# Performance work log

Measured on AMD Instinct MI355X. Metric: run time of the kernel, lower is better.

Reference implementation:

```python
import jax, jax.numpy as jnp
import numpy as np

NEG_SLOPE = 0.2  # PyG GATConv default negative_slope


def gat_conv(x, src, dst, W, a_src, a_dst, b, concat):
    # x: [N, F_in]; src/dst: [E] edge endpoints (edge j->i means src=j, dst=i)
    N = x.shape[0]
    H, C = a_src.shape
    xp = (x @ W).reshape(N, H, C)                      # per-head projection
    al_s = jnp.einsum('nhc,hc->nh', xp, a_src)          # source attention logits
    al_d = jnp.einsum('nhc,hc->nh', xp, a_dst)          # destination attention logits
    e = jax.nn.leaky_relu(al_s[src] + al_d[dst], NEG_SLOPE)   # [E, H]
    # segment softmax over incoming edges of each destination node
    m = jax.ops.segment_max(e, dst, num_segments=N)     # [N, H]
    m = jnp.where(jnp.isfinite(m), m, jnp.zeros_like(m))
    ex = jnp.exp(e - m[dst])
    den = jax.ops.segment_sum(ex, dst, num_segments=N)  # [N, H]
    alpha = ex / (den[dst] + 1e-16)                     # [E, H]
    out = jax.ops.segment_sum(xp[src] * alpha[:, :, None], dst, num_segments=N)  # [N,H,C]
    out = out.reshape(N, H * C) if concat else out.mean(axis=1)
    return out + b


def setup_inputs() -> dict:
    key = jax.random.key(0)
    ks = jax.random.split(key, 9)
    N, E, F_in, H, C = 50000, 1600000, 128, 4, 32
    x = jax.random.normal(ks[0], (N, F_in), dtype=jnp.float32)
    edge_index = jax.random.randint(ks[1], (2, E), 0, N, dtype=jnp.int64)
    s1 = 1.0 / np.sqrt(F_in)
    s2 = 1.0 / np.sqrt(H * C)
    return {
        'x': x,
        'edge_index': edge_index,
        'W1': jax.random.normal(ks[2], (F_in, H * C), dtype=jnp.float32) * s1,
        'a_src1': jax.random.normal(ks[3], (H, C), dtype=jnp.float32) * s1,
        'a_dst1': jax.random.normal(ks[4], (H, C), dtype=jnp.float32) * s1,
        'b1': jnp.zeros((H * C,), dtype=jnp.float32),
        'W2': jax.random.normal(ks[5], (H * C, C), dtype=jnp.float32) * s2,
        'a_src2': jax.random.normal(ks[6], (1, C), dtype=jnp.float32) * s2,
        'a_dst2': jax.random.normal(ks[7], (1, C), dtype=jnp.float32) * s2,
        'b2': jnp.zeros((C,), dtype=jnp.float32),
    }


def reference(x, edge_index, W1, a_src1, a_dst1, b1, W2, a_src2, a_dst2, b2):
    N = x.shape[0]
    loops = jnp.arange(N, dtype=edge_index.dtype)
    src = jnp.concatenate([edge_index[0], loops])   # PyG default add_self_loops=True
    dst = jnp.concatenate([edge_index[1], loops])
    h = gat_conv(x, src, dst, W1, a_src1, a_dst1, b1, concat=True)
    h = jax.nn.elu(h)
    out = gat_conv(h, src, dst, W2, a_src2, a_dst2, b2, concat=False)
    return out
```

## Files before the change

### kernel.cpp

```cpp
#include <hip/hip_runtime.h>
#include <hip/hip_fp16.h>

#define NEG_SLOPE 0.2f
#define CAP 128
#define NB  64
#define GAB 192

typedef __half half_t;

__device__ __forceinline__ float lrelu(float x) { return x >= 0.f ? x : NEG_SLOPE * x; }

__device__ __forceinline__ unsigned int f2h2(float a, float b) {
    union { unsigned int u; __half2 h; } v; v.h = __floats2half2_rn(a, b);
    return v.u;
}

__device__ __forceinline__ void fma8h(const uint4& v, float w, float* a) {
    const __half* hp = (const __half*)&v;
    #pragma unroll
    for (int j = 0; j < 8; ++j) a[j] = fmaf(w, __half2float(hp[j]), a[j]);
}

__device__ __forceinline__ bool edge_is64(const int* __restrict__ ei, int E) {
    int t = threadIdx.x & 63;
    int idx = 2 * t + 1; if (idx >= 2 * E) idx = 2 * E - 1;
    unsigned long long b = __ballot(ei[idx] != 0);
    return b == 0ULL;
}

__device__ __forceinline__ void load_edge(const int* __restrict__ ei, int E, int i,
                                          bool is64, int& s, int& d) {
    if (i < E) {
        if (is64) { const long long* e = (const long long*)ei; s = (int)e[i]; d = (int)e[E + i]; }
        else      { s = ei[i]; d = ei[E + i]; }
    } else { s = d = i - E; }
}

__global__ __launch_bounds__(256) void gemm1cnt_kernel(const float* __restrict__ x,
        const float* __restrict__ W1, const float* __restrict__ a_src,
        const float* __restrict__ a_dst, half_t* __restrict__ xp1h,
        float* __restrict__ al_s, float* __restrict__ al_d,
        const int* __restrict__ ei, int* __restrict__ partials,
        unsigned int* __restrict__ epacked, int N, int E, int shift, int G1) {
    __shared__ __align__(16) float xst[64 * 128];
    __shared__ __align__(16) float ws[64 * 128];
    int t = threadIdx.x;
    if (blockIdx.x >= G1) {
        int* cnts = (int*)xst;
        int b2 = blockIdx.x - G1;
        if (t < NB) cnts[t] = 0;
        bool is64 = edge_is64(ei, E);
        __syncthreads();
        int tot = E + N;
        for (int i = b2 * 256 + t; i < tot; i += GAB * 256) {
            int s, d; load_edge(ei, E, i, is64, s, d);
            epacked[i] = ((unsigned int)d << 16) | (unsigned int)s;
            atomicAdd(&cnts[d >> shift], 1);
        }
        __syncthreads();
        if (t < NB) partials[b2 * NB + t] = cnts[t];
        return;
    }
    int row0 = blockIdx.x * 128;
    int cg = t & 15, rg = t >> 4;
    float acc[8][8] = {};
    for (int chunk = 0; chunk < 2; ++chunk) {
        __syncthreads();
        int c0 = chunk * 64;
        #pragma unroll
        for (int ii = 0; ii < 8; ++ii) {
            int idx = t + 256 * ii;
            int r = idx >> 4, kq = idx & 15;
            int n = row0 + r;
            float4 v = make_float4(0.f, 0.f, 0.f, 0.f);
            if (n < N) v = *(const float4*)&x[(size_t)n * 128 + c0 + kq * 4];
            float vv[4] = {v.x, v.y, v.z, v.w};
            #pragma unroll
            for (int j = 0; j < 4; ++j) {
                int k = kq * 4 + j;
                xst[k * 128 + (((r >> 2) ^ (k & 31)) << 2) + (r & 3)] = vv[j];
            }
        }
        #pragma unroll
        for (int ii = 0; ii < 8; ++ii) {
            int idx = t + 256 * ii;
            int k = idx >> 5, cq = idx & 31;
            *(float4*)&ws[k * 128 + cq * 4] =
                *(const float4*)&W1[(size_t)(c0 + k) * 128 + cq * 4];
        }
        __syncthreads();
        int g0 = rg * 2, g1 = rg * 2 + 1;
        #pragma unroll 4
        for (int k = 0; k < 64; ++k) {
            int kb = k & 31;
            float4 xv0 = *(const float4*)&xst[k * 128 + ((g0 ^ kb) << 2)];
            float4 xv1 = *(const float4*)&xst[k * 128 + ((g1 ^ kb) << 2)];
            float4 wv0 = *(const float4*)&ws[k * 128 + cg * 8];
            float4 wv1 = *(const float4*)&ws[k * 128 + cg * 8 + 4];
            float xr[8] = {xv0.x, xv0.y, xv0.z, xv0.w, xv1.x, xv1.y, xv1.z, xv1.w};
            float wr[8] = {wv0.x, wv0.y, wv0.z, wv0.w, wv1.x, wv1.y, wv1.z, wv1.w};
            #pragma unroll
            for (int r = 0; r < 8; ++r)
                #pragma unroll
                for (int c = 0; c < 8; ++c)
                    acc[r][c] = fmaf(xr[r], wr[c], acc[r][c]);
        }
    }
    #pragma unroll
    for (int r = 0; r < 8; ++r) {
        int n = row0 + rg * 8 + r;
        if (n < N) {
            uint4 u = make_uint4(f2h2(acc[r][0], acc[r][1]), f2h2(acc[r][2], acc[r][3]),
                                 f2h2(acc[r][4], acc[r][5]), f2h2(acc[r][6], acc[r][7]));
            *(uint4*)&xp1h[(size_t)n * 128 + cg * 8] = u;
        }
    }
    float ps[8], pd[8];
    #pragma unroll
    for (int r = 0; r < 8; ++r) {
        float s = 0.f, dd = 0.f;
        #pragma unroll
        for (int c = 0; c < 8; ++c) {
            s  = fmaf(acc[r][c], a_src[cg * 8 + c], s);
            dd = fmaf(acc[r][c], a_dst[cg * 8 + c], dd);
        }
        ps[r] = s; pd[r] = dd;
    }
    #pragma unroll
    for (int m = 1; m < 4; m <<= 1) {
        #pragma unroll
        for (int r = 0; r < 8; ++r) { ps[r] += __shfl_xor(ps[r], m); pd[r] += __shfl_xor(pd[r], m); }
    }
    if ((cg & 3) == 0) {
        int head = cg >> 2;
        #pragma unroll
        for (int r = 0; r < 8; ++r) {
            int n = row0 + rg * 8 + r;
            if (n < N) { al_s[n * 4 + head] = ps[r]; al_d[n * 4 + head] = pd[r]; }
        }
    }
}

__global__ __launch_bounds__(256) void k_bin(const unsigned int* __restrict__ epacked,
        const int* __restrict__ partials, unsigned int* __restrict__ binned,
        int tot, int shift) {
    __shared__ int cur[NB];
    int t = threadIdx.x, b = blockIdx.x;
    if (t < NB) {
        int full = 0, pre = 0;
        for (int b2 = 0; b2 < GAB; ++b2) {
            int v = partials[b2 * NB + t];
            if (b2 < b) pre += v;
            full += v;
        }
        int incl = full;
        #pragma unroll
        for (int m = 1; m < 64; m <<= 1) {
            int u = __shfl_up(incl, m);
            if (t >= m) incl += u;
        }
        cur[t] = (incl - full) + pre;
    }
    __syncthreads();
    unsigned int mask = (1u << shift) - 1u;
    for (int i = b * 256 + t; i < tot; i += GAB * 256) {
        unsigned int e = epacked[i];
        unsigned int d = e >> 16;
        int pos = atomicAdd(&cur[d >> shift], 1);
        binned[pos] = ((d & mask) << 16) | (e & 0xFFFFu);
    }
}

__global__ __launch_bounds__(1024) void k_part(const unsigned int* __restrict__ binned,
        const int* __restrict__ partials, int* __restrict__ off, int* __restrict__ csr,
        int N, int shift) {
    __shared__ int cnt_loc[1024];
    __shared__ int scan_loc[1024];
    __shared__ int wsum[16];
    __shared__ int lo_s, hi_s;
    int b = blockIdx.x, t = threadIdx.x;
    int base = b << shift;
    int span = 1 << shift;
    if (t < 64) {
        int full = 0;
        for (int b2 = 0; b2 < GAB; ++b2) full += partials[b2 * NB + t];
        int incl = full;
        #pragma unroll
        for (int m = 1; m < 64; m <<= 1) {
            int u = __shfl_up(incl, m);
            if (t >= m) incl += u;
        }
        int excl = incl - full;
        int lov = __shfl(excl, b);
        int hiv = __shfl(incl, b);
        if (t == 0) { lo_s = lov; hi_s = hiv; }
    }
    if (t < span) cnt_loc[t] = 0;
    __syncthreads();
    int lo = lo_s, hi = hi_s;
    for (int i = lo + t; i < hi; i += 1024)
        atomicAdd(&cnt_loc[binned[i] >> 16], 1);
    __syncthreads();
    int v = (t < span) ? cnt_loc[t] : 0;
    int lane = t & 63, w = t >> 6;
    int incl = v;
    #pragma unroll
    for (int m = 1; m < 64; m <<= 1) {
        int u = __shfl_up(incl, m);
        if (lane >= m) incl += u;
    }
    if (lane == 63) wsum[w] = incl;
    __syncthreads();
    if (t == 0) {
        int run = 0;
        #pragma unroll
        for (int i2 = 0; i2 < 16; ++i2) { int s2 = wsum[i2]; wsum[i2] = run; run += s2; }
    }
    __syncthreads();
    int excl = incl - v + wsum[w];
    if (t < span) { scan_loc[t] = lo + excl; off[base + t] = lo + excl; }
    __syncthreads();
    if (t < span) cnt_loc[t] = 0;
    __syncthreads();
    for (int i = lo + t; i < hi; i += 1024) {
        unsigned int e = binned[i];
        int r = e >> 16;
        int pos = scan_loc[r] + atomicAdd(&cnt_loc[r], 1);
        csr[pos] = (int)(e & 0xFFFFu);
    }
}

__global__ __launch_bounds__(256) void edge1_kernel(const int* __restrict__ off,
        const int* __restrict__ csr, const float* __restrict__ al_s,
        const float* __restrict__ al_d, const half_t* __restrict__ xp1h,
        const float* __restrict__ b1, half_t* __restrict__ h1h, int N) {
    __shared__ int   srcs[4][CAP];
    __shared__ float ew[4][CAP * 4];
    int t = threadIdx.x;
    int wid = t >> 6, lane = t & 63;
    int d = blockIdx.x * 4 + wid;
    if (d >= N) return;
    int o0 = off[d], o1 = off[d + 1];
    int deg = o1 - o0; if (deg > CAP) deg = CAP;
    float4 ad = *(const float4*)&al_d[d * 4];
    float4 ex0 = make_float4(0.f, 0.f, 0.f, 0.f);
    float4 ex1 = make_float4(0.f, 0.f, 0.f, 0.f);
    if (lane < deg) {
        int s = csr[o0 + lane];
        srcs[wid][lane] = s << 4;
        float4 as = *(const float4*)&al_s[s * 4];
        ex0.x = __expf(lrelu(as.x + ad.x));
        ex0.y = __expf(lrelu(as.y + ad.y));
        ex0.z = __expf(lrelu(as.z + ad.z));
        ex0.w = __expf(lrelu(as.w + ad.w));
    }
    if (lane + 64 < deg) {
        int s = csr[o0 + lane + 64];
        srcs[wid][lane + 64] = s << 4;
        float4 as = *(const float4*)&al_s[s * 4];
        ex1.x = __expf(lrelu(as.x + ad.x));
        ex1.y = __expf(lrelu(as.y + ad.y));
        ex1.z = __expf(lrelu(as.z + ad.z));
        ex1.w = __expf(lrelu(as.w + ad.w));
    }
    float4 r = make_float4(ex0.x + ex1.x, ex0.y + ex1.y, ex0.z + ex1.z, ex0.w + ex1.w);
    #pragma unroll
    for (int m = 1; m < 64; m <<= 1) {
        r.x += __shfl_xor(r.x, m); r.y += __shfl_xor(r.y, m);
        r.z += __shfl_xor(r.z, m); r.w += __shfl_xor(r.w, m);
    }
    float4 ri = make_float4(1.f / (r.x + 1e-16f), 1.f / (r.y + 1e-16f),
                            1.f / (r.z + 1e-16f), 1.f / (r.w + 1e-16f));
    if (lane < deg)
        *(float4*)&ew[wid][lane * 4] =
            make_float4(ex0.x * ri.x, ex0.y * ri.y, ex0.z * ri.z, ex0.w * ri.w);
    if (lane + 64 < deg)
        *(float4*)&ew[wid][(lane + 64) * 4] =
            make_float4(ex1.x * ri.x, ex1.y * ri.y, ex1.z * ri.z, ex1.w * ri.w);
    int q = lane & 15, p = lane >> 4, h = q >> 2;
    float a[8] = {};
    const uint4* xr = (const uint4*)xp1h;
    for (int ib = p; ib < deg; ib += 16) {
        int i1 = ib + 4, i2 = ib + 8, i3 = ib + 12;
        bool c1 = i1 < deg, c2 = i2 < deg, c3 = i3 < deg;
        float w0 = ew[wid][ib * 4 + h];
        uint4 v0 = xr[(size_t)(srcs[wid][ib] + q)];
        float w1, w2, w3;
        uint4 v1, v2, v3;
        if (c1) { w1 = ew[wid][i1 * 4 + h]; v1 = xr[(size_t)(srcs[wid][i1] + q)]; }
        if (c2) { w2 = ew[wid][i2 * 4 + h]; v2 = xr[(size_t)(srcs[wid][i2] + q)]; }
        if (c3) { w3 = ew[wid][i3 * 4 + h]; v3 = xr[(size_t)(srcs[wid][i3] + q)]; }
        fma8h(v0, w0, a);
        if (c1) fma8h(v1, w1, a);
        if (c2) fma8h(v2, w2, a);
        if (c3) fma8h(v3, w3, a);
    }
    #pragma unroll
    for (int j = 0; j < 8; ++j) {
        a[j] += __shfl_xor(a[j], 16);
        a[j] += __shfl_xor(a[j], 32);
    }
    if (p == 0) {
        float4 b0 = *(const float4*)&b1[q * 8];
        float4 b4 = *(const float4*)&b1[q * 8 + 4];
        float v0 = a[0] + b0.x, v1 = a[1] + b0.y, v2 = a[2] + b0.z, v3 = a[3] + b0.w;
        float v4 = a[4] + b4.x, v5 = a[5] + b4.y, v6 = a[6] + b4.z, v7 = a[7] + b4.w;
        v0 = v0 > 0.f ? v0 : expm1f(v0);
        v1 = v1 > 0.f ? v1 : expm1f(v1);
        v2 = v2 > 0.f ? v2 : expm1f(v2);
        v3 = v3 > 0.f ? v3 : expm1f(v3);
        v4 = v4 > 0.f ? v4 : expm1f(v4);
        v5 = v5 > 0.f ? v5 : expm1f(v5);
        v6 = v6 > 0.f ? v6 : expm1f(v6);
        v7 = v7 > 0.f ? v7 : expm1f(v7);
        uint4 u = make_uint4(f2h2(v0, v1), f2h2(v2, v3), f2h2(v4, v5), f2h2(v6, v7));
        *(uint4*)&h1h[(size_t)d * 128 + q * 8] = u;
    }
}

__global__ __launch_bounds__(256) void gemm2l_kernel(const half_t* __restrict__ h1h,
        const float* __restrict__ W2, const float* __restrict__ a_s2,
        const float* __restrict__ a_d2, half_t* __restrict__ xp2h,
        float* __restrict__ al_s2, float* __restrict__ al_d2, int N) {
    __shared__ __align__(16) float w2s[128 * 32];
    int t = threadIdx.x;
    #pragma unroll
    for (int ii = 0; ii < 4; ++ii)
        ((float4*)w2s)[t + 256 * ii] = ((const float4*)W2)[t + 256 * ii];
    if (blockIdx.x == 0 && t < 2)
        ((uint4*)(xp2h + (size_t)N * 32))[t] = make_uint4(0, 0, 0, 0);
    __syncthreads();
    int n = blockIdx.x * 64 + (t >> 2), sub = t & 3;
    if (n >= N) return;
    const uint4* hr = (const uint4*)(h1h + (size_t)n * 128);
    float acc[8] = {};
    #pragma unroll 2
    for (int kq = 0; kq < 16; ++kq) {
        uint4 hv = hr[kq];
        const __half* hp = (const __half*)&hv;
        #pragma unroll
        for (int jj = 0; jj < 8; ++jj) {
            float h = __half2float(hp[jj]);
            int k = kq * 8 + jj;
            float4 wa = *(const float4*)&w2s[k * 32 + sub * 8];
            float4 wb = *(const float4*)&w2s[k * 32 + sub * 8 + 4];
            acc[0] = fmaf(h, wa.x, acc[0]); acc[1] = fmaf(h, wa.y, acc[1]);
            acc[2] = fmaf(h, wa.z, acc[2]); acc[3] = fmaf(h, wa.w, acc[3]);
            acc[4] = fmaf(h, wb.x, acc[4]); acc[5] = fmaf(h, wb.y, acc[5]);
            acc[6] = fmaf(h, wb.z, acc[6]); acc[7] = fmaf(h, wb.w, acc[7]);
        }
    }
    uint4 u = make_uint4(f2h2(acc[0], acc[1]), f2h2(acc[2], acc[3]),
                         f2h2(acc[4], acc[5]), f2h2(acc[6], acc[7]));
    *(uint4*)&xp2h[(size_t)n * 32 + sub * 8] = u;
    float ps = 0.f, pd = 0.f;
    #pragma unroll
    for (int c = 0; c < 8; ++c) {
        ps = fmaf(acc[c], a_s2[sub * 8 + c], ps);
        pd = fmaf(acc[c], a_d2[sub * 8 + c], pd);
    }
    ps += __shfl_xor(ps, 1); ps += __shfl_xor(ps, 2);
    pd += __shfl_xor(pd, 1); pd += __shfl_xor(pd, 2);
    if (sub == 0) { al_s2[n] = ps; al_d2[n] = pd; }
}

__global__ __launch_bounds__(256) void edge2_kernel(const int* __restrict__ off,
        const int* __restrict__ csr, const float* __restrict__ al_s,
        const float* __restrict__ al_d, const half_t* __restrict__ xp2h,
        const float* __restrict__ b2v, float* __restrict__ out, int N) {
    __shared__ int   srcs[4][CAP];
    __shared__ float ew[4][CAP];
    int t = threadIdx.x;
    int wid = t >> 6, lane = t & 63;
    int d = blockIdx.x * 4 + wid;
    if (d >= N) return;
    int o0 = off[d], o1 = off[d + 1];
    int deg = o1 - o0; if (deg > CAP) deg = CAP;
    float adv = al_d[d];
    float ex0 = 0.f, ex1 = 0.f;
    if (lane < deg) {
        int s = csr[o0 + lane];
        srcs[wid][lane] = s << 2;
        ex0 = __expf(lrelu(al_s[s] + adv));
    }
    if (lane + 64 < deg) {
        int s = csr[o0 + lane + 64];
        srcs[wid][lane + 64] = s << 2;
        ex1 = __expf(lrelu(al_s[s] + adv));
    }
    float r = ex0 + ex1;
    #pragma unroll
    for (int m = 1; m < 64; m <<= 1) r += __shfl_xor(r, m);
    float rinv = 1.f / (r + 1e-16f);
    if (lane < deg)      ew[wid][lane]      = ex0 * rinv;
    if (lane + 64 < deg) ew[wid][lane + 64] = ex1 * rinv;
    int q = lane & 3, p = lane >> 2;
    float a[8] = {};
    const uint4* xr = (const uint4*)xp2h;
    for (int ib = p; ib < deg; ib += 64) {
        int i1 = ib + 16, i2 = ib + 32, i3 = ib + 48;
        bool c1 = i1 < deg, c2 = i2 < deg, c3 = i3 < deg;
        float w0 = ew[wid][ib];
        uint4 v0 = xr[(size_t)(srcs[wid][ib] + q)];
        float w1, w2, w3;
        uint4 v1, v2, v3;
        if (c1) { w1 = ew[wid][i1]; v1 = xr[(size_t)(srcs[wid][i1] + q)]; }
        if (c2) { w2 = ew[wid][i2]; v2 = xr[(size_t)(srcs[wid][i2] + q)]; }
        if (c3) { w3 = ew[wid][i3]; v3 = xr[(size_t)(srcs[wid][i3] + q)]; }
        fma8h(v0, w0, a);
        if (c1) fma8h(v1, w1, a);
        if (c2) fma8h(v2, w2, a);
        if (c3) fma8h(v3, w3, a);
    }
    #pragma unroll
    for (int j = 0; j < 8; ++j) {
        a[j] += __shfl_xor(a[j], 4);
        a[j] += __shfl_xor(a[j], 8);
        a[j] += __shfl_xor(a[j], 16);
        a[j] += __shfl_xor(a[j], 32);
    }
    if (p == 0) {
        float4 b0 = *(const float4*)&b2v[q * 8];
        float4 b4 = *(const float4*)&b2v[q * 8 + 4];
        float4 o0v = make_float4(a[0] + b0.x, a[1] + b0.y, a[2] + b0.z, a[3] + b0.w);
        float4 o1v = make_float4(a[4] + b4.x, a[5] + b4.y, a[6] + b4.z, a[7] + b4.w);
        *(float4*)&out[(size_t)d * 32 + q * 8]     = o0v;
        *(float4*)&out[(size_t)d * 32 + q * 8 + 4] = o1v;
    }
}

extern "C" void kernel_launch(void* const* d_in, const int* in_sizes, int n_in,
                              void* d_out, int out_size, void* d_ws, size_t ws_size,
                              hipStream_t stream) {
    const float* x    = (const float*)d_in[0];
    const int*   ei   = (const int*)d_in[1];
    const float* W1   = (const float*)d_in[2];
    const float* a_s1 = (const float*)d_in[3];
    const float* a_d1 = (const float*)d_in[4];
    const float* b1   = (const float*)d_in[5];
    const float* W2   = (const float*)d_in[6];
    const float* a_s2 = (const float*)d_in[7];
    const float* a_d2 = (const float*)d_in[8];
    const float* b2   = (const float*)d_in[9];
    int N = in_sizes[0] / 128;
    int E = in_sizes[1] / 2;
    float* out = (float*)d_out;

    int shift = 0;
    while (((N - 1) >> shift) >= NB) shift++;

    char* wsb = (char*)d_ws;
    size_t off_b = 0;
    auto alloc = [&](size_t bytes) -> void* {
        void* p = wsb + off_b;
        off_b = (off_b + bytes + 255) & ~(size_t)255;
        return p;
    };
    int*          partials = (int*)          alloc((size_t)GAB * NB * 4);
    unsigned int* epacked  = (unsigned int*) alloc((size_t)(E + N) * 4);
    unsigned int* binned   = (unsigned int*) alloc((size_t)(E + N) * 4);
    int*          offs     = (int*)          alloc(((size_t)NB << shift) * 4 + 8);
    int*          csr      = (int*)          alloc((size_t)(E + N) * 4);
    half_t*       xp1h     = (half_t*)       alloc((size_t)(N + 1) * 128 * 2);
    float*        al_s1    = (float*)        alloc((size_t)N * 4 * 4);
    float*        al_d1    = (float*)        alloc((size_t)N * 4 * 4);
    half_t*       h1h      = (half_t*)       alloc((size_t)N * 128 * 2);
    half_t*       xp2h     = (half_t*)       alloc((size_t)(N + 1) * 32 * 2);
    float*        al_s2    = (float*)        alloc((size_t)N * 4);
    float*        al_d2    = (float*)        alloc((size_t)N * 4);

    int G1 = (N + 127) / 128;

    gemm1cnt_kernel<<<G1 + GAB, 256, 0, stream>>>(x, W1, a_s1, a_d1, xp1h, al_s1, al_d1,
                                                  ei, partials, epacked, N, E, shift, G1);
    k_bin<<<GAB, 256, 0, stream>>>(epacked, partials, binned, E + N, shift);
    k_part<<<NB, 1024, 0, stream>>>(binned, partials, offs, csr, N, shift);
    edge1_kernel<<<(N + 3) / 4, 256, 0, stream>>>(offs, csr, al_s1, al_d1, xp1h, b1, h1h, N);
    gemm2l_kernel<<<(N + 63) / 64, 256, 0, stream>>>(h1h, W2, a_s2, a_d2, xp2h, al_s2, al_d2, N);
    edge2_kernel<<<(N + 3) / 4, 256, 0, stream>>>(offs, csr, al_s2, al_d2, xp2h, b2, out, N);
}
```

Measured before the change: 269.5 us.

## Split layer-1 gather by head with head-planar projected features

Stores the layer-1 projected features in a head-planar layout (4 planes of N×32 halves) and launches the edge aggregation as four head-phases, each gathering only 64 bytes per source. Each head-phase is handled by a contiguous range of blocks, which keeps that head's 3.2 MB plane small enough to stay cache-resident and makes the random gathers more likely to hit. In exchange, the CSR offsets, source indices and softmax logits are re-read four times, and there is a larger cross-lane reduction. The ELU also swaps expm1f for __expf(x)-1, which loses some accuracy near zero.

```diff
diff --git a/kernel.cpp b/kernel.cpp
--- a/kernel.cpp
+++ b/kernel.cpp
@@ -38,7 +38,7 @@
 
 __global__ __launch_bounds__(256) void gemm1cnt_kernel(const float* __restrict__ x,
         const float* __restrict__ W1, const float* __restrict__ a_src,
-        const float* __restrict__ a_dst, half_t* __restrict__ xp1h,
+        const float* __restrict__ a_dst, half_t* __restrict__ xp1p,
         float* __restrict__ al_s, float* __restrict__ al_d,
         const int* __restrict__ ei, int* __restrict__ partials,
         unsigned int* __restrict__ epacked, int N, int E, int shift, int G1) {
@@ -112,7 +112,7 @@
         if (n < N) {
             uint4 u = make_uint4(f2h2(acc[r][0], acc[r][1]), f2h2(acc[r][2], acc[r][3]),
                                  f2h2(acc[r][4], acc[r][5]), f2h2(acc[r][6], acc[r][7]));
-            *(uint4*)&xp1h[(size_t)n * 128 + cg * 8] = u;
+            *(uint4*)&xp1p[(size_t)(cg >> 2) * N * 32 + (size_t)n * 32 + (cg & 3) * 8] = u;
         }
     }
     float ps[8], pd[8];
@@ -230,66 +230,50 @@
     }
 }
 
-__global__ __launch_bounds__(256) void edge1_kernel(const int* __restrict__ off,
+__global__ __launch_bounds__(256) void edge1p_kernel(const int* __restrict__ off,
         const int* __restrict__ csr, const float* __restrict__ al_s,
-        const float* __restrict__ al_d, const half_t* __restrict__ xp1h,
-        const float* __restrict__ b1, half_t* __restrict__ h1h, int N) {
+        const float* __restrict__ al_d, const half_t* __restrict__ xp1p,
+        const float* __restrict__ b1, half_t* __restrict__ h1h, int N, int PB) {
     __shared__ int   srcs[4][CAP];
-    __shared__ float ew[4][CAP * 4];
+    __shared__ float ew[4][CAP];
     int t = threadIdx.x;
     int wid = t >> 6, lane = t & 63;
-    int d = blockIdx.x * 4 + wid;
+    int ph = blockIdx.x / PB;
+    int d = (blockIdx.x - ph * PB) * 4 + wid;
     if (d >= N) return;
     int o0 = off[d], o1 = off[d + 1];
     int deg = o1 - o0; if (deg > CAP) deg = CAP;
-    float4 ad = *(const float4*)&al_d[d * 4];
-    float4 ex0 = make_float4(0.f, 0.f, 0.f, 0.f);
-    float4 ex1 = make_float4(0.f, 0.f, 0.f, 0.f);
+    float adv = al_d[d * 4 + ph];
+    float ex0 = 0.f, ex1 = 0.f;
     if (lane < deg) {
         int s = csr[o0 + lane];
-        srcs[wid][lane] = s << 4;
-        float4 as = *(const float4*)&al_s[s * 4];
-        ex0.x = __expf(lrelu(as.x + ad.x));
-        ex0.y = __expf(lrelu(as.y + ad.y));
-        ex0.z = __expf(lrelu(as.z + ad.z));
-        ex0.w = __expf(lrelu(as.w + ad.w));
+        srcs[wid][lane] = s << 2;
+        ex0 = __expf(lrelu(al_s[s * 4 + ph] + adv));
     }
     if (lane + 64 < deg) {
         int s = csr[o0 + lane + 64];
-        srcs[wid][lane + 64] = s << 4;
-        float4 as = *(const float4*)&al_s[s * 4];
-        ex1.x = __expf(lrelu(as.x + ad.x));
-        ex1.y = __expf(lrelu(as.y + ad.y));
-        ex1.z = __expf(lrelu(as.z + ad.z));
-        ex1.w = __expf(lrelu(as.w + ad.w));
-    }
-    float4 r = make_float4(ex0.x + ex1.x, ex0.y + ex1.y, ex0.z + ex1.z, ex0.w + ex1.w);
-    #pragma unroll
-    for (int m = 1; m < 64; m <<= 1) {
-        r.x += __shfl_xor(r.x, m); r.y += __shfl_xor(r.y, m);
-        r.z += __shfl_xor(r.z, m); r.w += __shfl_xor(r.w, m);
-    }
-    float4 ri = make_float4(1.f / (r.x + 1e-16f), 1.f / (r.y + 1e-16f),
-                            1.f / (r.z + 1e-16f), 1.f / (r.w + 1e-16f));
-    if (lane < deg)
-        *(float4*)&ew[wid][lane * 4] =
-            make_float4(ex0.x * ri.x, ex0.y * ri.y, ex0.z * ri.z, ex0.w * ri.w);
-    if (lane + 64 < deg)
-        *(float4*)&ew[wid][(lane + 64) * 4] =
-            make_float4(ex1.x * ri.x, ex1.y * ri.y, ex1.z * ri.z, ex1.w * ri.w);
-    int q = lane & 15, p = lane >> 4, h = q >> 2;
+        srcs[wid][lane + 64] = s << 2;
+        ex1 = __expf(lrelu(al_s[s * 4 + ph] + adv));
+    }
+    float r = ex0 + ex1;
+    #pragma unroll
+    for (int m = 1; m < 64; m <<= 1) r += __shfl_xor(r, m);
+    float rinv = 1.f / (r + 1e-16f);
+    if (lane < deg)      ew[wid][lane]      = ex0 * rinv;
+    if (lane + 64 < deg) ew[wid][lane + 64] = ex1 * rinv;
+    int q = lane & 3, p = lane >> 2;
     float a[8] = {};
-    const uint4* xr = (const uint4*)xp1h;
-    for (int ib = p; ib < deg; ib += 16) {
-        int i1 = ib + 4, i2 = ib + 8, i3 = ib + 12;
+    const uint4* xr = (const uint4*)xp1p + (size_t)ph * N * 4;
+    for (int ib = p; ib < deg; ib += 64) {
+        int i1 = ib + 16, i2 = ib + 32, i3 = ib + 48;
         bool c1 = i1 < deg, c2 = i2 < deg, c3 = i3 < deg;
-        float w0 = ew[wid][ib * 4 + h];
+        float w0 = ew[wid][ib];
         uint4 v0 = xr[(size_t)(srcs[wid][ib] + q)];
         float w1, w2, w3;
         uint4 v1, v2, v3;
-        if (c1) { w1 = ew[wid][i1 * 4 + h]; v1 = xr[(size_t)(srcs[wid][i1] + q)]; }
-        if (c2) { w2 = ew[wid][i2 * 4 + h]; v2 = xr[(size_t)(srcs[wid][i2] + q)]; }
-        if (c3) { w3 = ew[wid][i3 * 4 + h]; v3 = xr[(size_t)(srcs[wid][i3] + q)]; }
+        if (c1) { w1 = ew[wid][i1]; v1 = xr[(size_t)(srcs[wid][i1] + q)]; }
+        if (c2) { w2 = ew[wid][i2]; v2 = xr[(size_t)(srcs[wid][i2] + q)]; }
+        if (c3) { w3 = ew[wid][i3]; v3 = xr[(size_t)(srcs[wid][i3] + q)]; }
         fma8h(v0, w0, a);
         if (c1) fma8h(v1, w1, a);
         if (c2) fma8h(v2, w2, a);
@@ -297,24 +281,27 @@
     }
     #pragma unroll
     for (int j = 0; j < 8; ++j) {
+        a[j] += __shfl_xor(a[j], 4);
+        a[j] += __shfl_xor(a[j], 8);
         a[j] += __shfl_xor(a[j], 16);
         a[j] += __shfl_xor(a[j], 32);
     }
     if (p == 0) {
-        float4 b0 = *(const float4*)&b1[q * 8];
-        float4 b4 = *(const float4*)&b1[q * 8 + 4];
+        int cb = ph * 32 + q * 8;
+        float4 b0 = *(const float4*)&b1[cb];
+        float4 b4 = *(const float4*)&b1[cb + 4];
         float v0 = a[0] + b0.x, v1 = a[1] + b0.y, v2 = a[2] + b0.z, v3 = a[3] + b0.w;
         float v4 = a[4] + b4.x, v5 = a[5] + b4.y, v6 = a[6] + b4.z, v7 = a[7] + b4.w;
-        v0 = v0 > 0.f ? v0 : expm1f(v0);
-        v1 = v1 > 0.f ? v1 : expm1f(v1);
-        v2 = v2 > 0.f ? v2 : expm1f(v2);
-        v3 = v3 > 0.f ? v3 : expm1f(v3);
-        v4 = v4 > 0.f ? v4 : expm1f(v4);
-        v5 = v5 > 0.f ? v5 : expm1f(v5);
-        v6 = v6 > 0.f ? v6 : expm1f(v6);
-        v7 = v7 > 0.f ? v7 : expm1f(v7);
+        v0 = v0 > 0.f ? v0 : __expf(v0) - 1.f;
+        v1 = v1 > 0.f ? v1 : __expf(v1) - 1.f;
+        v2 = v2 > 0.f ? v2 : __expf(v2) - 1.f;
+        v3 = v3 > 0.f ? v3 : __expf(v3) - 1.f;
+        v4 = v4 > 0.f ? v4 : __expf(v4) - 1.f;
+        v5 = v5 > 0.f ? v5 : __expf(v5) - 1.f;
+        v6 = v6 > 0.f ? v6 : __expf(v6) - 1.f;
+        v7 = v7 > 0.f ? v7 : __expf(v7) - 1.f;
         uint4 u = make_uint4(f2h2(v0, v1), f2h2(v2, v3), f2h2(v4, v5), f2h2(v6, v7));
-        *(uint4*)&h1h[(size_t)d * 128 + q * 8] = u;
+        *(uint4*)&h1h[(size_t)d * 128 + cb] = u;
     }
 }
 
@@ -461,7 +448,7 @@
     unsigned int* binned   = (unsigned int*) alloc((size_t)(E + N) * 4);
     int*          offs     = (int*)          alloc(((size_t)NB << shift) * 4 + 8);
     int*          csr      = (int*)          alloc((size_t)(E + N) * 4);
-    half_t*       xp1h     = (half_t*)       alloc((size_t)(N + 1) * 128 * 2);
+    half_t*       xp1p     = (half_t*)       alloc((size_t)4 * N * 32 * 2);
     float*        al_s1    = (float*)        alloc((size_t)N * 4 * 4);
     float*        al_d1    = (float*)        alloc((size_t)N * 4 * 4);
     half_t*       h1h      = (half_t*)       alloc((size_t)N * 128 * 2);
@@ -470,12 +457,13 @@
     float*        al_d2    = (float*)        alloc((size_t)N * 4);
 
     int G1 = (N + 127) / 128;
-
-    gemm1cnt_kernel<<<G1 + GAB, 256, 0, stream>>>(x, W1, a_s1, a_d1, xp1h, al_s1, al_d1,
+    int PB = (N + 3) / 4;
+
+    gemm1cnt_kernel<<<G1 + GAB, 256, 0, stream>>>(x, W1, a_s1, a_d1, xp1p, al_s1, al_d1,
                                                   ei, partials, epacked, N, E, shift, G1);
     k_bin<<<GAB, 256, 0, stream>>>(epacked, partials, binned, E + N, shift);
     k_part<<<NB, 1024, 0, stream>>>(binned, partials, offs, csr, N, shift);
-    edge1_kernel<<<(N + 3) / 4, 256, 0, stream>>>(offs, csr, al_s1, al_d1, xp1h, b1, h1h, N);
+    edge1p_kernel<<<4 * PB, 256, 0, stream>>>(offs, csr, al_s1, al_d1, xp1p, b1, h1h, N, PB);
     gemm2l_kernel<<<(N + 63) / 64, 256, 0, stream>>>(h1h, W2, a_s2, a_d2, xp2h, al_s2, al_d2, N);
     edge2_kernel<<<(N + 3) / 4, 256, 0, stream>>>(offs, csr, al_s2, al_d2, xp2h, b2, out, N);
 }
```

New measurement: 317.5 us. 1.18x slower.

## Increase CSR build bucket count to 256 to spread partition work

Applied to the files above, without the earlier changes.

Raises the number of destination buckets from 64 to 256, so the per-bucket partition kernel launches 256 blocks of 1024 threads instead of 64, each handling a smaller node span. The prefix scans in the binning and partition kernels become multi-wave (256-entry) scans, and k_part now gets the total edge count to bound the last bucket. This targets low GPU occupancy in the CSR construction stage. In exchange it adds more partial-count traffic (GAB×256 reads per block) and assumes the shift computed elsewhere makes the span fit within 1024.

```diff
diff --git a/kernel.cpp b/kernel.cpp
--- a/kernel.cpp
+++ b/kernel.cpp
@@ -3,7 +3,7 @@
 
 #define NEG_SLOPE 0.2f
 #define CAP 128
-#define NB  64
+#define NB  256
 #define GAB 192
 
 typedef __half half_t;
@@ -145,22 +145,27 @@
         const int* __restrict__ partials, unsigned int* __restrict__ binned,
         int tot, int shift) {
     __shared__ int cur[NB];
+    __shared__ int wsc[4];
     int t = threadIdx.x, b = blockIdx.x;
-    if (t < NB) {
-        int full = 0, pre = 0;
-        for (int b2 = 0; b2 < GAB; ++b2) {
-            int v = partials[b2 * NB + t];
-            if (b2 < b) pre += v;
-            full += v;
-        }
-        int incl = full;
-        #pragma unroll
-        for (int m = 1; m < 64; m <<= 1) {
-            int u = __shfl_up(incl, m);
-            if (t >= m) incl += u;
-        }
-        cur[t] = (incl - full) + pre;
-    }
+    int full = 0, pre = 0;
+    for (int b2 = 0; b2 < GAB; ++b2) {
+        int v = partials[b2 * NB + t];
+        if (b2 < b) pre += v;
+        full += v;
+    }
+    int lane = t & 63, w = t >> 6;
+    int incl = full;
+    #pragma unroll
+    for (int m = 1; m < 64; m <<= 1) {
+        int u = __shfl_up(incl, m);
+        if (lane >= m) incl += u;
+    }
+    if (lane == 63) wsc[w] = incl;
+    __syncthreads();
+    int wpre = 0;
+    #pragma unroll
+    for (int i = 0; i < 4; ++i) if (i < w) wpre += wsc[i];
+    cur[t] = (incl - full) + wpre + pre;
     __syncthreads();
     unsigned int mask = (1u << shift) - 1u;
     for (int i = b * 256 + t; i < tot; i += GAB * 256) {
@@ -173,31 +178,39 @@
 
 __global__ __launch_bounds__(1024) void k_part(const unsigned int* __restrict__ binned,
         const int* __restrict__ partials, int* __restrict__ off, int* __restrict__ csr,
-        int N, int shift) {
+        int N, int shift, int tot) {
     __shared__ int cnt_loc[1024];
     __shared__ int scan_loc[1024];
     __shared__ int wsum[16];
-    __shared__ int lo_s, hi_s;
+    __shared__ int bf[NB];
     int b = blockIdx.x, t = threadIdx.x;
     int base = b << shift;
     int span = 1 << shift;
-    if (t < 64) {
+    if (t < NB) {
         int full = 0;
         for (int b2 = 0; b2 < GAB; ++b2) full += partials[b2 * NB + t];
-        int incl = full;
+        bf[t] = full;
+    }
+    __syncthreads();
+    if (t < 64) {
+        int s0 = bf[4 * t], s1 = bf[4 * t + 1], s2 = bf[4 * t + 2], s3 = bf[4 * t + 3];
+        int sum4 = s0 + s1 + s2 + s3;
+        int incl = sum4;
         #pragma unroll
         for (int m = 1; m < 64; m <<= 1) {
             int u = __shfl_up(incl, m);
             if (t >= m) incl += u;
         }
-        int excl = incl - full;
-        int lov = __shfl(excl, b);
-        int hiv = __shfl(incl, b);
-        if (t == 0) { lo_s = lov; hi_s = hiv; }
+        int excl = incl - sum4;
+        bf[4 * t] = excl;
+        bf[4 * t + 1] = excl + s0;
+        bf[4 * t + 2] = excl + s0 + s1;
+        bf[4 * t + 3] = excl + s0 + s1 + s2;
     }
     if (t < span) cnt_loc[t] = 0;
     __syncthreads();
-    int lo = lo_s, hi = hi_s;
+    int lo = bf[b];
+    int hi = (b == NB - 1) ? tot : bf[b + 1];
     for (int i = lo + t; i < hi; i += 1024)
         atomicAdd(&cnt_loc[binned[i] >> 16], 1);
     __syncthreads();
@@ -474,7 +487,7 @@
     gemm1cnt_kernel<<<G1 + GAB, 256, 0, stream>>>(x, W1, a_s1, a_d1, xp1h, al_s1, al_d1,
                                                   ei, partials, epacked, N, E, shift, G1);
     k_bin<<<GAB, 256, 0, stream>>>(epacked, partials, binned, E + N, shift);
-    k_part<<<NB, 1024, 0, stream>>>(binned, partials, offs, csr, N, shift);
+    k_part<<<NB, 1024, 0, stream>>>(binned, partials, offs, csr, N, shift, E + N);
     edge1_kernel<<<(N + 3) / 4, 256, 0, stream>>>(offs, csr, al_s1, al_d1, xp1h, b1, h1h, N);
     gemm2l_kernel<<<(N + 63) / 64, 256, 0, stream>>>(h1h, W2, a_s2, a_d2, xp2h, al_s2, al_d2, N);
     edge2_kernel<<<(N + 3) / 4, 256, 0, stream>>>(offs, csr, al_s2, al_d2, xp2h, b2, out, N);
```

Result: faster. 257.4 us (median of 2 runs) (-4.5%).
